# Kernel tuning notes

Measured on AMD Instinct MI355X. Metric: run time of the kernel, lower is better.

## Reference

```python
import jax, jax.numpy as jnp
import numpy as np

GROUP_SIZE = 128
INTERMEDIATE = 18944


def _unpack_int4(packed):
    # packed: [rows, cols//8] int32, 8 nibbles per int32 along output dim
    shifts = jnp.arange(8, dtype=jnp.int32) * 4
    nib = (packed[:, :, None] >> shifts) & 15  # [rows, cols//8, 8]
    return nib.reshape(packed.shape[0], packed.shape[1] * 8)


def awq_gemm(x, qweight, qzeros, scales, group_size):
    # Dequantize: W[i,j] = (w4[i,j] - z4[i//g, j]) * scales[i//g, j]
    w = _unpack_int4(qweight).astype(jnp.float32)           # [in, out]
    z = _unpack_int4(qzeros).astype(jnp.float32)            # [in//g, out]
    s = scales.astype(jnp.float32)                          # [in//g, out]
    W = ((w - jnp.repeat(z, group_size, axis=0)) * jnp.repeat(s, group_size, axis=0))
    return (x @ W.astype(x.dtype))                          # [tokens, out]


def setup_inputs() -> dict:
    key = jax.random.key(0)
    ks = jax.random.split(key, 7)
    imax = 2147483647
    return {
        "x": (jax.random.normal(ks[0], (4096, 3584), dtype=jnp.float32) * 0.02).astype(jnp.float16),
        "qweight_gu": jax.random.randint(ks[1], (3584, 4736), 0, imax, dtype=jnp.int32),
        "qzeros_gu": jax.random.randint(ks[2], (28, 4736), 0, imax, dtype=jnp.int32),
        "scales_gu": (jax.random.uniform(ks[3], (28, 37888), dtype=jnp.float32) * 0.01 + 0.001).astype(jnp.float16),
        "qweight_down": jax.random.randint(ks[4], (18944, 448), 0, imax, dtype=jnp.int32),
        "qzeros_down": jax.random.randint(ks[5], (148, 448), 0, imax, dtype=jnp.int32),
        "scales_down": (jax.random.uniform(ks[6], (148, 3584), dtype=jnp.float32) * 0.01 + 0.001).astype(jnp.float16),
    }


def reference(x, qweight_gu, qzeros_gu, scales_gu, qweight_down, qzeros_down, scales_down):
    # Fused gate+up AWQ GEMM (matches forward path after fuse_gate_up())
    gate_up = awq_gemm(x, qweight_gu, qzeros_gu, scales_gu, GROUP_SIZE)  # [T, 2*I]
    gate = gate_up[..., :INTERMEDIATE]
    up = gate_up[..., INTERMEDIATE:]
    intermediate = jax.nn.silu(gate) * up                                # fused SiLU*mul
    down = awq_gemm(intermediate, qweight_down, qzeros_down, scales_down, GROUP_SIZE)
    return down
```

## Files before the change

kernel.cpp:

```cpp
#include <hip/hip_runtime.h>
#include <hip/hip_fp16.h>
#include <stdint.h>

typedef _Float16 half8 __attribute__((ext_vector_type(8)));
typedef _Float16 h2v __attribute__((ext_vector_type(2)));
typedef float f32x4 __attribute__((ext_vector_type(4)));

#define GLD_LDS16(gp, lp)                                                     \
  __builtin_amdgcn_global_load_lds(                                           \
      (const __attribute__((address_space(1))) void*)(gp),                    \
      (__attribute__((address_space(3))) void*)(lp), 16, 0, 0)
#define GLD_LDS4(gp, lp)                                                      \
  __builtin_amdgcn_global_load_lds(                                           \
      (const __attribute__((address_space(1))) void*)(gp),                    \
      (__attribute__((address_space(3))) void*)(lp), 4, 0, 0)

__global__ void xcvt_kernel(const float* __restrict__ in, __half* __restrict__ out) {
  const size_t i = ((size_t)blockIdx.x * 256 + threadIdx.x) * 4;
  float4 v = *(const float4*)(in + i);
  __half2* o = (__half2*)(out + i);
  o[0] = __floats2half2_rn(v.x, v.y);
  o[1] = __floats2half2_rn(v.z, v.w);
}

__global__ void repack_kernel(const int* __restrict__ qw, uint32_t* __restrict__ rp, int P) {
  const int N = P * 8;
  const int n = blockIdx.x * 256 + threadIdx.x;
  const int j8 = n >> 3;
  const int sh = (n & 7) * 4;
  #pragma unroll
  for (int qi = 0; qi < 4; ++qi) {
    const int q = blockIdx.y * 4 + qi;
    const int* src = qw + (size_t)(q * 8) * P + j8;
    uint32_t r = 0;
    #pragma unroll
    for (int t = 0; t < 8; ++t) {
      uint32_t w = ((uint32_t)src[t * P] >> sh) & 15u;
      r |= w << (4 * (t >> 1) + 16 * (t & 1));
    }
    rp[(size_t)q * N + n] = r;
  }
}

__global__ void smz_kernel(const float* __restrict__ sc, const int* __restrict__ qz,
                           uint32_t* __restrict__ smz, int P) {
  const int N = P * 8;
  const int n = blockIdx.x * 256 + threadIdx.x;
  const int g = blockIdx.y;
  uint32_t sbits = __half_as_ushort(__float2half(sc[(size_t)g * N + n]));
  uint32_t z = ((uint32_t)qz[(size_t)g * P + (n >> 3)] >> ((n & 7) * 4)) & 15u;
  uint32_t hz = 0x6400u | z;
  smz[(size_t)g * N + n] = sbits | (hz << 16);
}

union U32H2 { uint32_t u; h2v h; };
__device__ inline h2v bith2(uint32_t u) { U32H2 t; t.u = u; return t.h; }
__device__ inline uint32_t h2bit(h2v h) { U32H2 t; t.h = h; return t.u; }
__device__ inline half8 dequant8(uint32_t p, h2v s, h2v z) {
  union { uint32_t u[4]; half8 v; } r;
  r.u[0] = h2bit((bith2((p & 0x000F000Fu) | 0x64006400u) - z) * s);
  r.u[1] = h2bit((bith2(((p >> 4) & 0x000F000Fu) | 0x64006400u) - z) * s);
  r.u[2] = h2bit((bith2(((p >> 8) & 0x000F000Fu) | 0x64006400u) - z) * s);
  r.u[3] = h2bit((bith2(((p >> 12) & 0x000F000Fu) | 0x64006400u) - z) * s);
  return r.v;
}

template <int KDIM, int NW, int T1OFF, int OW, bool SILU, int BXS>
__global__ __launch_bounds__(512, 4) void awq_gemm(const __half* __restrict__ A,
                                                   const uint32_t* __restrict__ RP,
                                                   const uint32_t* __restrict__ SMZ,
                                                   void* __restrict__ OUT) {
  constexpr int ABUF = 128 * 64 * 2;
  constexpr int BBUF = 8 * 256 * 4;
  constexpr int BOFF = 3 * ABUF;
  constexpr int ZOFF = BOFF + 3 * BBUF;
  __shared__ __align__(16) unsigned char smem[ZOFF + 2048];

  const int tid = threadIdx.x;
  const int l = tid & 63;
  const int wv = tid >> 6;
  const int l15 = l & 15;
  const int l4 = l >> 4;
  const int wc = wv * 16;

  const int row0 = blockIdx.y * 128;
  const int n0 = blockIdx.x * BXS;

  const __half* asrc[2];
  #pragma unroll
  for (int it = 0; it < 2; ++it) {
    int m = it * 64 + (tid >> 3);
    int cs = tid & 7;
    int kc = cs ^ (m & 7);
    asrc[it] = A + (size_t)(row0 + m) * KDIM + kc * 8;
  }

  const uint32_t* bsrc;
  {
    int qr = tid >> 6;
    int c4 = (tid & 63) * 4;
    int S = ((qr & 1) << 4) | ((qr >> 1) << 2);
    int cS = c4 ^ S;
    int bcol = (cS < 128) ? n0 + cS : n0 + T1OFF + (cS - 128);
    bsrc = RP + (size_t)qr * NW + bcol;
  }

  const uint32_t* zsrc;
  {
    int w3 = wv & 3;
    int zc = w3 * 64 + l;
    zsrc = SMZ + ((zc < 128) ? n0 + zc : n0 + T1OFF + (zc - 128));
  }
  const int zdst = ZOFF + (wv & 3) * 256;

  f32x4 acc0[8], acc1[8];
  const f32x4 zero4 = {0.f, 0.f, 0.f, 0.f};
  #pragma unroll
  for (int mf = 0; mf < 8; ++mf) { acc0[mf] = zero4; acc1[mf] = zero4; }

  uint32_t s2[2], z2[2];
  constexpr int NSTEP = KDIM / 64;

  #pragma unroll
  for (int it = 0; it < 2; ++it)
    GLD_LDS16(asrc[it], &smem[it * 8192 + tid * 16]);
  GLD_LDS16(bsrc, &smem[BOFF + tid * 16]);
  GLD_LDS4(zsrc, &smem[zdst]);
  #pragma unroll
  for (int it = 0; it < 2; ++it)
    GLD_LDS16(asrc[it] + 64, &smem[ABUF + it * 8192 + tid * 16]);
  GLD_LDS16(bsrc + (size_t)8 * NW, &smem[BOFF + BBUF + tid * 16]);

  int cur = 0, stg = 2;
  for (int t = 0; t < NSTEP; ++t) {
    if (t == NSTEP - 1)      asm volatile("s_waitcnt vmcnt(0)" ::: "memory");
    else if (t & 1)          asm volatile("s_waitcnt vmcnt(4)" ::: "memory");
    else                     asm volatile("s_waitcnt vmcnt(3)" ::: "memory");
    __builtin_amdgcn_s_barrier();

    if (t + 2 < NSTEP) {
      #pragma unroll
      for (int it = 0; it < 2; ++it)
        GLD_LDS16(asrc[it] + (size_t)(t + 2) * 64,
                  &smem[stg * ABUF + it * 8192 + tid * 16]);
      GLD_LDS16(bsrc + (size_t)(t + 2) * 8 * NW, &smem[BOFF + stg * BBUF + tid * 16]);
      if (((t + 2) & 1) == 0) {
        const int g = (t + 2) >> 1;
        GLD_LDS4(zsrc + (size_t)g * NW, &smem[zdst + (g & 1) * 1024]);
      }
    }

    if ((t & 1) == 0) {
      const uint32_t* zl = (const uint32_t*)&smem[ZOFF + ((t >> 1) & 1) * 1024];
      uint32_t u0 = zl[wc + l15];
      uint32_t u1 = zl[128 + wc + l15];
      uint32_t lo0 = u0 & 0xFFFFu, lo1 = u1 & 0xFFFFu;
      s2[0] = lo0 | (lo0 << 16);
      z2[0] = (u0 & 0xFFFF0000u) | (u0 >> 16);
      s2[1] = lo1 | (lo1 << 16);
      z2[1] = (u1 & 0xFFFF0000u) | (u1 >> 16);
    }

    uint32_t bq[2][2];
    const uint32_t* bdw = (const uint32_t*)&smem[BOFF + cur * BBUF];
    #pragma unroll
    for (int kk = 0; kk < 2; ++kk) {
      const int Sl = ((l4 & 1) << 4) | (kk << 3) | ((l4 >> 1) << 2);
      const int qrow = (kk * 4 + l4) * 256;
      bq[kk][0] = bdw[qrow + ((wc + l15) ^ Sl)];
      bq[kk][1] = bdw[qrow + ((128 + wc + l15) ^ Sl)];
    }

    const unsigned char* abase = &smem[cur * ABUF];
    __builtin_amdgcn_s_setprio(1);
    #pragma unroll
    for (int kk = 0; kk < 2; ++kk) {
      half8 b0 = dequant8(bq[kk][0], bith2(s2[0]), bith2(z2[0]));
      half8 b1 = dequant8(bq[kk][1], bith2(s2[1]), bith2(z2[1]));
      const int chunkoff = ((kk * 4 + l4) ^ (l15 & 7)) * 16;
      #pragma unroll
      for (int mf = 0; mf < 8; ++mf) {
        half8 a = *(const half8*)(abase + (mf * 16 + l15) * 128 + chunkoff);
        acc0[mf] = __builtin_amdgcn_mfma_f32_16x16x32_f16(a, b0, acc0[mf], 0, 0, 0);
        acc1[mf] = __builtin_amdgcn_mfma_f32_16x16x32_f16(a, b1, acc1[mf], 0, 0, 0);
      }
    }
    __builtin_amdgcn_s_setprio(0);

    cur = (cur == 2) ? 0 : cur + 1;
    stg = (stg == 2) ? 0 : stg + 1;
  }

  if (SILU) {
    __half* O = (__half*)OUT;
    #pragma unroll
    for (int mf = 0; mf < 8; ++mf)
      #pragma unroll
      for (int r = 0; r < 4; ++r) {
        int row = row0 + mf * 16 + l4 * 4 + r;
        int col = n0 + wc + l15;
        float gf = __half2float(__float2half(acc0[mf][r]));
        float uf = __half2float(__float2half(acc1[mf][r]));
        float sig = 1.f / (1.f + __expf(-gf));
        float sil = __half2float(__float2half(gf * sig));
        O[(size_t)row * OW + col] = __float2half(sil * uf);
      }
  } else {
    float* O = (float*)OUT;
    #pragma unroll
    for (int mf = 0; mf < 8; ++mf)
      #pragma unroll
      for (int r = 0; r < 4; ++r) {
        int row = row0 + mf * 16 + l4 * 4 + r;
        int col0 = n0 + wc + l15;
        int col1 = n0 + T1OFF + wc + l15;
        O[(size_t)row * OW + col0] = __half2float(__float2half(acc0[mf][r]));
        O[(size_t)row * OW + col1] = __half2float(__float2half(acc1[mf][r]));
      }
  }
}

extern "C" void kernel_launch(void* const* d_in, const int* in_sizes, int n_in,
                              void* d_out, int out_size, void* d_ws, size_t ws_size,
                              hipStream_t stream) {
  const float* x_f32 = (const float*)d_in[0];
  const int* qw_gu = (const int*)d_in[1];
  const int* qz_gu = (const int*)d_in[2];
  const float* sc_gu = (const float*)d_in[3];
  const int* qw_dn = (const int*)d_in[4];
  const int* qz_dn = (const int*)d_in[5];
  const float* sc_dn = (const float*)d_in[6];

  char* ws = (char*)d_ws;
  __half* interm   = (__half*)ws;
  uint32_t* rp_gu  = (uint32_t*)(ws + 155189248ull);
  uint32_t* smz_gu = (uint32_t*)(ws + 223084544ull);
  __half* xh       = (__half*)(ws + 227328000ull);
  uint32_t* rp_dn  = (uint32_t*)(ws + 155189248ull);
  uint32_t* smz_dn = (uint32_t*)(ws + 189136896ull);

  xcvt_kernel<<<14336, 256, 0, stream>>>(x_f32, xh);
  repack_kernel<<<dim3(148, 112), 256, 0, stream>>>(qw_gu, rp_gu, 4736);
  smz_kernel<<<dim3(148, 28), 256, 0, stream>>>(sc_gu, qz_gu, smz_gu, 4736);

  awq_gemm<3584, 37888, 18944, 18944, true, 128>
      <<<dim3(148, 32), 512, 0, stream>>>(xh, rp_gu, smz_gu, (void*)interm);

  repack_kernel<<<dim3(14, 592), 256, 0, stream>>>(qw_dn, rp_dn, 448);
  smz_kernel<<<dim3(14, 148), 256, 0, stream>>>(sc_dn, qz_dn, smz_dn, 448);

  awq_gemm<18944, 3584, 128, 3584, false, 256>
      <<<dim3(14, 32), 512, 0, stream>>>(interm, rp_dn, smz_dn, d_out);
}
```

Baseline: 1.630 ms.

## Enlarge M tile to 256 with 2x4 warp grid and phased barrier pipeline

Doubles the block's M tile to 256 rows and arranges the 8 warps as 2x4, each computing a 128x64 tile with 32 accumulators. Each dequantized weight fragment is reused across more MFMAs, which cuts dequant ALU work and LDS traffic per FLOP. The K-step is split into four barrier-separated phases that interleave global-to-LDS prefetch with MFMA work. The cost is higher register pressure (launch bounds lowered to 2 blocks/CU), more barriers, and half as many blocks, which may underfill the GPU for the down projection.

```diff
diff --git a/kernel.cpp b/kernel.cpp
--- a/kernel.cpp
+++ b/kernel.cpp
@@ -14,6 +14,8 @@
   __builtin_amdgcn_global_load_lds(                                           \
       (const __attribute__((address_space(1))) void*)(gp),                    \
       (__attribute__((address_space(3))) void*)(lp), 4, 0, 0)
+
+#define SBAR() asm volatile("s_barrier" ::: "memory")
 
 __global__ void xcvt_kernel(const float* __restrict__ in, __half* __restrict__ out) {
   const size_t i = ((size_t)blockIdx.x * 256 + threadIdx.x) * 4;
@@ -66,11 +68,11 @@
 }
 
 template <int KDIM, int NW, int T1OFF, int OW, bool SILU, int BXS>
-__global__ __launch_bounds__(512, 4) void awq_gemm(const __half* __restrict__ A,
+__global__ __launch_bounds__(512, 2) void awq_gemm(const __half* __restrict__ A,
                                                    const uint32_t* __restrict__ RP,
                                                    const uint32_t* __restrict__ SMZ,
                                                    void* __restrict__ OUT) {
-  constexpr int ABUF = 128 * 64 * 2;
+  constexpr int ABUF = 256 * 64 * 2;
   constexpr int BBUF = 8 * 256 * 4;
   constexpr int BOFF = 3 * ABUF;
   constexpr int ZOFF = BOFF + 3 * BBUF;
@@ -79,16 +81,18 @@
   const int tid = threadIdx.x;
   const int l = tid & 63;
   const int wv = tid >> 6;
+  const int wm = wv >> 2;
+  const int wn = wv & 3;
   const int l15 = l & 15;
   const int l4 = l >> 4;
-  const int wc = wv * 16;
-
-  const int row0 = blockIdx.y * 128;
+  const int l157 = l15 & 7;
+
+  const int row0 = blockIdx.y * 256;
   const int n0 = blockIdx.x * BXS;
 
-  const __half* asrc[2];
-  #pragma unroll
-  for (int it = 0; it < 2; ++it) {
+  const __half* asrc[4];
+  #pragma unroll
+  for (int it = 0; it < 4; ++it) {
     int m = it * 64 + (tid >> 3);
     int cs = tid & 7;
     int kc = cs ^ (m & 7);
@@ -107,85 +111,141 @@
 
   const uint32_t* zsrc;
   {
-    int w3 = wv & 3;
-    int zc = w3 * 64 + l;
+    int zc = tid & 255;
     zsrc = SMZ + ((zc < 128) ? n0 + zc : n0 + T1OFF + (zc - 128));
   }
-  const int zdst = ZOFF + (wv & 3) * 256;
-
-  f32x4 acc0[8], acc1[8];
+
+  int chi[4];
+  #pragma unroll
+  for (int nf = 0; nf < 4; ++nf)
+    chi[nf] = (nf >> 1) * 128 + wn * 32 + (nf & 1) * 16 + l15;
+  int arow[8];
+  #pragma unroll
+  for (int mf = 0; mf < 8; ++mf)
+    arow[mf] = (wm * 128 + mf * 16 + l15) * 128;
+
+  f32x4 acc[4][8];
   const f32x4 zero4 = {0.f, 0.f, 0.f, 0.f};
   #pragma unroll
-  for (int mf = 0; mf < 8; ++mf) { acc0[mf] = zero4; acc1[mf] = zero4; }
-
-  uint32_t s2[2], z2[2];
+  for (int nf = 0; nf < 4; ++nf)
+    #pragma unroll
+    for (int mf = 0; mf < 8; ++mf) acc[nf][mf] = zero4;
+
+  uint32_t s2[4], z2[4];
   constexpr int NSTEP = KDIM / 64;
 
   #pragma unroll
-  for (int it = 0; it < 2; ++it)
+  for (int it = 0; it < 4; ++it)
     GLD_LDS16(asrc[it], &smem[it * 8192 + tid * 16]);
   GLD_LDS16(bsrc, &smem[BOFF + tid * 16]);
-  GLD_LDS4(zsrc, &smem[zdst]);
-  #pragma unroll
-  for (int it = 0; it < 2; ++it)
+  GLD_LDS4(zsrc, &smem[ZOFF + (tid & 255) * 4]);
+  #pragma unroll
+  for (int it = 0; it < 4; ++it)
     GLD_LDS16(asrc[it] + 64, &smem[ABUF + it * 8192 + tid * 16]);
   GLD_LDS16(bsrc + (size_t)8 * NW, &smem[BOFF + BBUF + tid * 16]);
 
+  asm volatile("s_waitcnt vmcnt(5)" ::: "memory");
+  SBAR();
+
   int cur = 0, stg = 2;
   for (int t = 0; t < NSTEP; ++t) {
-    if (t == NSTEP - 1)      asm volatile("s_waitcnt vmcnt(0)" ::: "memory");
-    else if (t & 1)          asm volatile("s_waitcnt vmcnt(4)" ::: "memory");
-    else                     asm volatile("s_waitcnt vmcnt(3)" ::: "memory");
-    __builtin_amdgcn_s_barrier();
+    const int aoff = cur * ABUF;
+    uint32_t bq[4];
+    half8 afr[4], bfr[4];
+    const uint32_t* bdw = (const uint32_t*)&smem[BOFF + cur * BBUF];
+    const int Sl0 = ((l4 & 1) << 4) | ((l4 >> 1) << 2);
 
     if (t + 2 < NSTEP) {
-      #pragma unroll
-      for (int it = 0; it < 2; ++it)
-        GLD_LDS16(asrc[it] + (size_t)(t + 2) * 64,
-                  &smem[stg * ABUF + it * 8192 + tid * 16]);
+      GLD_LDS16(asrc[0] + (size_t)(t + 2) * 64, &smem[stg * ABUF + tid * 16]);
+      GLD_LDS16(asrc[1] + (size_t)(t + 2) * 64, &smem[stg * ABUF + 8192 + tid * 16]);
+    }
+    #pragma unroll
+    for (int nf = 0; nf < 4; ++nf)
+      bq[nf] = bdw[l4 * 256 + (chi[nf] ^ Sl0)];
+    if ((t & 1) == 0) {
+      const uint32_t* zl = (const uint32_t*)&smem[ZOFF + ((t >> 1) & 1) * 1024];
+      #pragma unroll
+      for (int nf = 0; nf < 4; ++nf) {
+        uint32_t u = zl[chi[nf]];
+        uint32_t lo = u & 0xFFFFu;
+        s2[nf] = lo | (lo << 16);
+        z2[nf] = (u & 0xFFFF0000u) | (u >> 16);
+      }
+    }
+    #pragma unroll
+    for (int i = 0; i < 4; ++i)
+      afr[i] = *(const half8*)&smem[aoff + arow[i] + (l4 ^ l157) * 16];
+    SBAR();
+    __builtin_amdgcn_s_setprio(1);
+    #pragma unroll
+    for (int nf = 0; nf < 4; ++nf)
+      bfr[nf] = dequant8(bq[nf], bith2(s2[nf]), bith2(z2[nf]));
+    #pragma unroll
+    for (int nf = 0; nf < 4; ++nf)
+      #pragma unroll
+      for (int i = 0; i < 4; ++i)
+        acc[nf][i] = __builtin_amdgcn_mfma_f32_16x16x32_f16(afr[i], bfr[nf], acc[nf][i], 0, 0, 0);
+    __builtin_amdgcn_s_setprio(0);
+    SBAR();
+
+    if (t + 2 < NSTEP) {
+      GLD_LDS16(asrc[2] + (size_t)(t + 2) * 64, &smem[stg * ABUF + 16384 + tid * 16]);
+      GLD_LDS16(asrc[3] + (size_t)(t + 2) * 64, &smem[stg * ABUF + 24576 + tid * 16]);
+    }
+    #pragma unroll
+    for (int i = 0; i < 4; ++i)
+      afr[i] = *(const half8*)&smem[aoff + arow[4 + i] + (l4 ^ l157) * 16];
+    SBAR();
+    __builtin_amdgcn_s_setprio(1);
+    #pragma unroll
+    for (int nf = 0; nf < 4; ++nf)
+      #pragma unroll
+      for (int i = 0; i < 4; ++i)
+        acc[nf][4 + i] = __builtin_amdgcn_mfma_f32_16x16x32_f16(afr[i], bfr[nf], acc[nf][4 + i], 0, 0, 0);
+    __builtin_amdgcn_s_setprio(0);
+    SBAR();
+
+    if (t + 2 < NSTEP) {
       GLD_LDS16(bsrc + (size_t)(t + 2) * 8 * NW, &smem[BOFF + stg * BBUF + tid * 16]);
       if (((t + 2) & 1) == 0) {
         const int g = (t + 2) >> 1;
-        GLD_LDS4(zsrc + (size_t)g * NW, &smem[zdst + (g & 1) * 1024]);
+        GLD_LDS4(zsrc + (size_t)g * NW, &smem[ZOFF + (g & 1) * 1024 + (tid & 255) * 4]);
       }
     }
-
-    if ((t & 1) == 0) {
-      const uint32_t* zl = (const uint32_t*)&smem[ZOFF + ((t >> 1) & 1) * 1024];
-      uint32_t u0 = zl[wc + l15];
-      uint32_t u1 = zl[128 + wc + l15];
-      uint32_t lo0 = u0 & 0xFFFFu, lo1 = u1 & 0xFFFFu;
-      s2[0] = lo0 | (lo0 << 16);
-      z2[0] = (u0 & 0xFFFF0000u) | (u0 >> 16);
-      s2[1] = lo1 | (lo1 << 16);
-      z2[1] = (u1 & 0xFFFF0000u) | (u1 >> 16);
-    }
-
-    uint32_t bq[2][2];
-    const uint32_t* bdw = (const uint32_t*)&smem[BOFF + cur * BBUF];
-    #pragma unroll
-    for (int kk = 0; kk < 2; ++kk) {
-      const int Sl = ((l4 & 1) << 4) | (kk << 3) | ((l4 >> 1) << 2);
-      const int qrow = (kk * 4 + l4) * 256;
-      bq[kk][0] = bdw[qrow + ((wc + l15) ^ Sl)];
-      bq[kk][1] = bdw[qrow + ((128 + wc + l15) ^ Sl)];
-    }
-
-    const unsigned char* abase = &smem[cur * ABUF];
+    #pragma unroll
+    for (int nf = 0; nf < 4; ++nf)
+      bq[nf] = bdw[(4 + l4) * 256 + (chi[nf] ^ (Sl0 | 8))];
+    #pragma unroll
+    for (int i = 0; i < 4; ++i)
+      afr[i] = *(const half8*)&smem[aoff + arow[i] + ((4 + l4) ^ l157) * 16];
+    SBAR();
     __builtin_amdgcn_s_setprio(1);
     #pragma unroll
-    for (int kk = 0; kk < 2; ++kk) {
-      half8 b0 = dequant8(bq[kk][0], bith2(s2[0]), bith2(z2[0]));
-      half8 b1 = dequant8(bq[kk][1], bith2(s2[1]), bith2(z2[1]));
-      const int chunkoff = ((kk * 4 + l4) ^ (l15 & 7)) * 16;
-      #pragma unroll
-      for (int mf = 0; mf < 8; ++mf) {
-        half8 a = *(const half8*)(abase + (mf * 16 + l15) * 128 + chunkoff);
-        acc0[mf] = __builtin_amdgcn_mfma_f32_16x16x32_f16(a, b0, acc0[mf], 0, 0, 0);
-        acc1[mf] = __builtin_amdgcn_mfma_f32_16x16x32_f16(a, b1, acc1[mf], 0, 0, 0);
-      }
-    }
+    for (int nf = 0; nf < 4; ++nf)
+      bfr[nf] = dequant8(bq[nf], bith2(s2[nf]), bith2(z2[nf]));
+    #pragma unroll
+    for (int nf = 0; nf < 4; ++nf)
+      #pragma unroll
+      for (int i = 0; i < 4; ++i)
+        acc[nf][i] = __builtin_amdgcn_mfma_f32_16x16x32_f16(afr[i], bfr[nf], acc[nf][i], 0, 0, 0);
     __builtin_amdgcn_s_setprio(0);
+    SBAR();
+
+    #pragma unroll
+    for (int i = 0; i < 4; ++i)
+      afr[i] = *(const half8*)&smem[aoff + arow[4 + i] + ((4 + l4) ^ l157) * 16];
+    SBAR();
+    __builtin_amdgcn_s_setprio(1);
+    #pragma unroll
+    for (int nf = 0; nf < 4; ++nf)
+      #pragma unroll
+      for (int i = 0; i < 4; ++i)
+        acc[nf][4 + i] = __builtin_amdgcn_mfma_f32_16x16x32_f16(afr[i], bfr[nf], acc[nf][4 + i], 0, 0, 0);
+    __builtin_amdgcn_s_setprio(0);
+    if (t + 2 >= NSTEP)      asm volatile("s_waitcnt vmcnt(0)" ::: "memory");
+    else if (t & 1)          asm volatile("s_waitcnt vmcnt(5)" ::: "memory");
+    else                     asm volatile("s_waitcnt vmcnt(6)" ::: "memory");
+    SBAR();
 
     cur = (cur == 2) ? 0 : cur + 1;
     stg = (stg == 2) ? 0 : stg + 1;
@@ -194,29 +254,31 @@
   if (SILU) {
     __half* O = (__half*)OUT;
     #pragma unroll
-    for (int mf = 0; mf < 8; ++mf)
-      #pragma unroll
-      for (int r = 0; r < 4; ++r) {
-        int row = row0 + mf * 16 + l4 * 4 + r;
-        int col = n0 + wc + l15;
-        float gf = __half2float(__float2half(acc0[mf][r]));
-        float uf = __half2float(__float2half(acc1[mf][r]));
-        float sig = 1.f / (1.f + __expf(-gf));
-        float sil = __half2float(__float2half(gf * sig));
-        O[(size_t)row * OW + col] = __float2half(sil * uf);
-      }
+    for (int nfg = 0; nfg < 2; ++nfg)
+      #pragma unroll
+      for (int mf = 0; mf < 8; ++mf)
+        #pragma unroll
+        for (int r = 0; r < 4; ++r) {
+          int row = row0 + wm * 128 + mf * 16 + l4 * 4 + r;
+          int col = n0 + wn * 32 + nfg * 16 + l15;
+          float gf = __half2float(__float2half(acc[nfg][mf][r]));
+          float uf = __half2float(__float2half(acc[2 + nfg][mf][r]));
+          float sig = 1.f / (1.f + __expf(-gf));
+          float sil = __half2float(__float2half(gf * sig));
+          O[(size_t)row * OW + col] = __float2half(sil * uf);
+        }
   } else {
     float* O = (float*)OUT;
     #pragma unroll
-    for (int mf = 0; mf < 8; ++mf)
-      #pragma unroll
-      for (int r = 0; r < 4; ++r) {
-        int row = row0 + mf * 16 + l4 * 4 + r;
-        int col0 = n0 + wc + l15;
-        int col1 = n0 + T1OFF + wc + l15;
-        O[(size_t)row * OW + col0] = __half2float(__float2half(acc0[mf][r]));
-        O[(size_t)row * OW + col1] = __half2float(__float2half(acc1[mf][r]));
-      }
+    for (int nf = 0; nf < 4; ++nf)
+      #pragma unroll
+      for (int mf = 0; mf < 8; ++mf)
+        #pragma unroll
+        for (int r = 0; r < 4; ++r) {
+          int row = row0 + wm * 128 + mf * 16 + l4 * 4 + r;
+          int col = n0 + (nf >> 1) * T1OFF + wn * 32 + (nf & 1) * 16 + l15;
+          O[(size_t)row * OW + col] = __half2float(__float2half(acc[nf][mf][r]));
+        }
   }
 }
 
@@ -244,11 +306,11 @@
   smz_kernel<<<dim3(148, 28), 256, 0, stream>>>(sc_gu, qz_gu, smz_gu, 4736);
 
   awq_gemm<3584, 37888, 18944, 18944, true, 128>
-      <<<dim3(148, 32), 512, 0, stream>>>(xh, rp_gu, smz_gu, (void*)interm);
+      <<<dim3(148, 16), 512, 0, stream>>>(xh, rp_gu, smz_gu, (void*)interm);
 
   repack_kernel<<<dim3(14, 592), 256, 0, stream>>>(qw_dn, rp_dn, 448);
   smz_kernel<<<dim3(14, 148), 256, 0, stream>>>(sc_dn, qz_dn, smz_dn, 448);
 
   awq_gemm<18944, 3584, 128, 3584, false, 256>
-      <<<dim3(14, 32), 512, 0, stream>>>(interm, rp_dn, smz_dn, d_out);
-}
+      <<<dim3(14, 16), 512, 0, stream>>>(interm, rp_dn, smz_dn, d_out);
+}
```

Result: slower. 1.820 ms (+11.6%).

## Use 256-row M tile for gate/up AWQ GEMM with 2x4 warp layout

Applied to the files above, without the earlier changes.

Adds an awq_gemm_big kernel that doubles the M tile to 256 rows and arranges the 8 waves as 2x4 (each wave covering 128 rows by 64 columns), and uses it for the gate/up GEMM with half as many row blocks. Each dequantized B fragment now feeds twice as many MFMAs, which cuts weight loads and dequant work per output and halves how often B is re-read from global memory. In exchange, LDS use and register pressure grow (32 accumulator vectors per lane, launch bounds lowered to 2 blocks per CU), so occupancy drops. The grid is also smaller, which may hurt load balance across CUs.

```diff
diff --git a/kernel.cpp b/kernel.cpp
--- a/kernel.cpp
+++ b/kernel.cpp
@@ -66,6 +66,180 @@
 }
 
 template <int KDIM, int NW, int T1OFF, int OW, bool SILU, int BXS>
+__global__ __launch_bounds__(512, 2) void awq_gemm_big(const __half* __restrict__ A,
+                                                       const uint32_t* __restrict__ RP,
+                                                       const uint32_t* __restrict__ SMZ,
+                                                       void* __restrict__ OUT) {
+  constexpr int ABUF = 256 * 64 * 2;
+  constexpr int BBUF = 8 * 256 * 4;
+  constexpr int BOFF = 3 * ABUF;
+  constexpr int ZOFF = BOFF + 3 * BBUF;
+  __shared__ __align__(16) unsigned char smem[ZOFF + 2048];
+
+  const int tid = threadIdx.x;
+  const int l = tid & 63;
+  const int wv = tid >> 6;
+  const int wm = wv >> 2;
+  const int wn = wv & 3;
+  const int l15 = l & 15;
+  const int l4 = l >> 4;
+  const int l157 = l15 & 7;
+
+  const int row0 = blockIdx.y * 256;
+  const int n0 = blockIdx.x * BXS;
+
+  const __half* asrc[4];
+  #pragma unroll
+  for (int it = 0; it < 4; ++it) {
+    int m = it * 64 + (tid >> 3);
+    int cs = tid & 7;
+    int kc = cs ^ (m & 7);
+    asrc[it] = A + (size_t)(row0 + m) * KDIM + kc * 8;
+  }
+
+  const uint32_t* bsrc;
+  {
+    int qr = tid >> 6;
+    int c4 = (tid & 63) * 4;
+    int S = ((qr & 1) << 4) | ((qr >> 1) << 2);
+    int cS = c4 ^ S;
+    int bcol = (cS < 128) ? n0 + cS : n0 + T1OFF + (cS - 128);
+    bsrc = RP + (size_t)qr * NW + bcol;
+  }
+
+  const uint32_t* zsrc;
+  {
+    int zc = tid & 255;
+    zsrc = SMZ + ((zc < 128) ? n0 + zc : n0 + T1OFF + (zc - 128));
+  }
+
+  int chi[4];
+  #pragma unroll
+  for (int nf = 0; nf < 4; ++nf)
+    chi[nf] = (nf >> 1) * 128 + wn * 32 + (nf & 1) * 16 + l15;
+  int arow[8];
+  #pragma unroll
+  for (int mf = 0; mf < 8; ++mf)
+    arow[mf] = (wm * 128 + mf * 16 + l15) * 128;
+
+  f32x4 acc[4][8];
+  const f32x4 zero4 = {0.f, 0.f, 0.f, 0.f};
+  #pragma unroll
+  for (int nf = 0; nf < 4; ++nf)
+    #pragma unroll
+    for (int mf = 0; mf < 8; ++mf) acc[nf][mf] = zero4;
+
+  uint32_t s2[4], z2[4];
+  constexpr int NSTEP = KDIM / 64;
+
+  #pragma unroll
+  for (int it = 0; it < 4; ++it)
+    GLD_LDS16(asrc[it], &smem[it * 8192 + tid * 16]);
+  GLD_LDS16(bsrc, &smem[BOFF + tid * 16]);
+  GLD_LDS4(zsrc, &smem[ZOFF + (tid & 255) * 4]);
+  #pragma unroll
+  for (int it = 0; it < 4; ++it)
+    GLD_LDS16(asrc[it] + 64, &smem[ABUF + it * 8192 + tid * 16]);
+  GLD_LDS16(bsrc + (size_t)8 * NW, &smem[BOFF + BBUF + tid * 16]);
+
+  int cur = 0, stg = 2;
+  for (int t = 0; t < NSTEP; ++t) {
+    if (t == NSTEP - 1)      asm volatile("s_waitcnt vmcnt(0)" ::: "memory");
+    else if (t & 1)          asm volatile("s_waitcnt vmcnt(6)" ::: "memory");
+    else                     asm volatile("s_waitcnt vmcnt(5)" ::: "memory");
+    __builtin_amdgcn_s_barrier();
+
+    if (t + 2 < NSTEP) {
+      #pragma unroll
+      for (int it = 0; it < 4; ++it)
+        GLD_LDS16(asrc[it] + (size_t)(t + 2) * 64,
+                  &smem[stg * ABUF + it * 8192 + tid * 16]);
+      GLD_LDS16(bsrc + (size_t)(t + 2) * 8 * NW, &smem[BOFF + stg * BBUF + tid * 16]);
+      if (((t + 2) & 1) == 0) {
+        const int g = (t + 2) >> 1;
+        GLD_LDS4(zsrc + (size_t)g * NW, &smem[ZOFF + (g & 1) * 1024 + (tid & 255) * 4]);
+      }
+    }
+
+    if ((t & 1) == 0) {
+      const uint32_t* zl = (const uint32_t*)&smem[ZOFF + ((t >> 1) & 1) * 1024];
+      #pragma unroll
+      for (int nf = 0; nf < 4; ++nf) {
+        uint32_t u = zl[chi[nf]];
+        uint32_t lo = u & 0xFFFFu;
+        s2[nf] = lo | (lo << 16);
+        z2[nf] = (u & 0xFFFF0000u) | (u >> 16);
+      }
+    }
+
+    uint32_t bq[2][4];
+    const uint32_t* bdw = (const uint32_t*)&smem[BOFF + cur * BBUF];
+    #pragma unroll
+    for (int kk = 0; kk < 2; ++kk) {
+      const int Sl = ((l4 & 1) << 4) | (kk << 3) | ((l4 >> 1) << 2);
+      #pragma unroll
+      for (int nf = 0; nf < 4; ++nf)
+        bq[kk][nf] = bdw[(kk * 4 + l4) * 256 + (chi[nf] ^ Sl)];
+    }
+
+    const unsigned char* abase = &smem[cur * ABUF];
+    __builtin_amdgcn_s_setprio(1);
+    #pragma unroll
+    for (int kk = 0; kk < 2; ++kk) {
+      const int coff = ((kk * 4 + l4) ^ l157) * 16;
+      half8 afr[8];
+      #pragma unroll
+      for (int mf = 0; mf < 8; ++mf)
+        afr[mf] = *(const half8*)&smem[(size_t)(abase - smem) + arow[mf] + coff];
+      half8 bfr[4];
+      #pragma unroll
+      for (int nf = 0; nf < 4; ++nf)
+        bfr[nf] = dequant8(bq[kk][nf], bith2(s2[nf]), bith2(z2[nf]));
+      #pragma unroll
+      for (int nf = 0; nf < 4; ++nf)
+        #pragma unroll
+        for (int mf = 0; mf < 8; ++mf)
+          acc[nf][mf] =
+              __builtin_amdgcn_mfma_f32_16x16x32_f16(afr[mf], bfr[nf], acc[nf][mf], 0, 0, 0);
+    }
+    __builtin_amdgcn_s_setprio(0);
+
+    cur = (cur == 2) ? 0 : cur + 1;
+    stg = (stg == 2) ? 0 : stg + 1;
+  }
+
+  if (SILU) {
+    __half* O = (__half*)OUT;
+    #pragma unroll
+    for (int nfg = 0; nfg < 2; ++nfg)
+      #pragma unroll
+      for (int mf = 0; mf < 8; ++mf)
+        #pragma unroll
+        for (int r = 0; r < 4; ++r) {
+          int row = row0 + wm * 128 + mf * 16 + l4 * 4 + r;
+          int col = n0 + wn * 32 + nfg * 16 + l15;
+          float gf = __half2float(__float2half(acc[nfg][mf][r]));
+          float uf = __half2float(__float2half(acc[2 + nfg][mf][r]));
+          float sig = 1.f / (1.f + __expf(-gf));
+          float sil = __half2float(__float2half(gf * sig));
+          O[(size_t)row * OW + col] = __float2half(sil * uf);
+        }
+  } else {
+    float* O = (float*)OUT;
+    #pragma unroll
+    for (int nf = 0; nf < 4; ++nf)
+      #pragma unroll
+      for (int mf = 0; mf < 8; ++mf)
+        #pragma unroll
+        for (int r = 0; r < 4; ++r) {
+          int row = row0 + wm * 128 + mf * 16 + l4 * 4 + r;
+          int col = n0 + (nf >> 1) * T1OFF + wn * 32 + (nf & 1) * 16 + l15;
+          O[(size_t)row * OW + col] = __half2float(__float2half(acc[nf][mf][r]));
+        }
+  }
+}
+
+template <int KDIM, int NW, int T1OFF, int OW, bool SILU, int BXS>
 __global__ __launch_bounds__(512, 4) void awq_gemm(const __half* __restrict__ A,
                                                    const uint32_t* __restrict__ RP,
                                                    const uint32_t* __restrict__ SMZ,
@@ -243,8 +417,8 @@
   repack_kernel<<<dim3(148, 112), 256, 0, stream>>>(qw_gu, rp_gu, 4736);
   smz_kernel<<<dim3(148, 28), 256, 0, stream>>>(sc_gu, qz_gu, smz_gu, 4736);
 
-  awq_gemm<3584, 37888, 18944, 18944, true, 128>
-      <<<dim3(148, 32), 512, 0, stream>>>(xh, rp_gu, smz_gu, (void*)interm);
+  awq_gemm_big<3584, 37888, 18944, 18944, true, 128>
+      <<<dim3(148, 16), 512, 0, stream>>>(xh, rp_gu, smz_gu, (void*)interm);
 
   repack_kernel<<<dim3(14, 592), 256, 0, stream>>>(qw_dn, rp_dn, 448);
   smz_kernel<<<dim3(14, 148), 256, 0, stream>>>(sc_dn, qz_dn, smz_dn, 448);
```

Measured after the change: 1.683 ms. 3.3% more time.

## Switch AWQ GEMM to 32x32x16 MFMA with k-major A layout in LDS

Applied to the files above, without the earlier changes.

Replaces the 16x16x32 MFMA tiling, where each wave covered 16 gate and 16 up columns, with 32x32x16 MFMA tiles where each wave owns 32 output columns. The A tile is stored in LDS in a k-chunk-major layout without the XOR swizzle, and the B and zero-point loads are simplified to match. Each wave now dequantizes fewer B values per step and does fewer, larger MFMAs. In exchange, the SiLU epilogue has to pass the up results through shared memory between waves with extra barriers. The unswizzled A layout may cause LDS bank conflicts.

```diff
diff --git a/kernel.cpp b/kernel.cpp
--- a/kernel.cpp
+++ b/kernel.cpp
@@ -4,7 +4,7 @@
 
 typedef _Float16 half8 __attribute__((ext_vector_type(8)));
 typedef _Float16 h2v __attribute__((ext_vector_type(2)));
-typedef float f32x4 __attribute__((ext_vector_type(4)));
+typedef float f32x16 __attribute__((ext_vector_type(16)));
 
 #define GLD_LDS16(gp, lp)                                                     \
   __builtin_amdgcn_global_load_lds(                                           \
@@ -70,7 +70,7 @@
                                                    const uint32_t* __restrict__ RP,
                                                    const uint32_t* __restrict__ SMZ,
                                                    void* __restrict__ OUT) {
-  constexpr int ABUF = 128 * 64 * 2;
+  constexpr int ABUF = 8 * 128 * 16;
   constexpr int BBUF = 8 * 256 * 4;
   constexpr int BOFF = 3 * ABUF;
   constexpr int ZOFF = BOFF + 3 * BBUF;
@@ -79,53 +79,48 @@
   const int tid = threadIdx.x;
   const int l = tid & 63;
   const int wv = tid >> 6;
-  const int l15 = l & 15;
-  const int l4 = l >> 4;
-  const int wc = wv * 16;
+  const int l31 = l & 31;
+  const int lh = l >> 5;
 
   const int row0 = blockIdx.y * 128;
   const int n0 = blockIdx.x * BXS;
 
   const __half* asrc[2];
   #pragma unroll
-  for (int it = 0; it < 2; ++it) {
-    int m = it * 64 + (tid >> 3);
-    int cs = tid & 7;
-    int kc = cs ^ (m & 7);
-    asrc[it] = A + (size_t)(row0 + m) * KDIM + kc * 8;
-  }
+  for (int it = 0; it < 2; ++it)
+    asrc[it] = A + (size_t)(row0 + (tid & 127)) * KDIM + (it * 4 + (tid >> 7)) * 8;
 
   const uint32_t* bsrc;
   {
     int qr = tid >> 6;
     int c4 = (tid & 63) * 4;
-    int S = ((qr & 1) << 4) | ((qr >> 1) << 2);
-    int cS = c4 ^ S;
-    int bcol = (cS < 128) ? n0 + cS : n0 + T1OFF + (cS - 128);
+    int bcol = (c4 < 128) ? n0 + c4 : n0 + T1OFF + (c4 - 128);
     bsrc = RP + (size_t)qr * NW + bcol;
   }
 
   const uint32_t* zsrc;
   {
-    int w3 = wv & 3;
-    int zc = w3 * 64 + l;
+    int zc = tid & 255;
     zsrc = SMZ + ((zc < 128) ? n0 + zc : n0 + T1OFF + (zc - 128));
   }
-  const int zdst = ZOFF + (wv & 3) * 256;
-
-  f32x4 acc0[8], acc1[8];
-  const f32x4 zero4 = {0.f, 0.f, 0.f, 0.f};
-  #pragma unroll
-  for (int mf = 0; mf < 8; ++mf) { acc0[mf] = zero4; acc1[mf] = zero4; }
-
-  uint32_t s2[2], z2[2];
+
+  f32x16 acc[4];
+  #pragma unroll
+  for (int rf = 0; rf < 4; ++rf)
+    #pragma unroll
+    for (int e = 0; e < 16; ++e) acc[rf][e] = 0.f;
+
+  uint32_t s2, z2;
   constexpr int NSTEP = KDIM / 64;
+
+  const int bidx = wv * 32 + l31;
+  const int arow16 = l31 * 16;
 
   #pragma unroll
   for (int it = 0; it < 2; ++it)
     GLD_LDS16(asrc[it], &smem[it * 8192 + tid * 16]);
   GLD_LDS16(bsrc, &smem[BOFF + tid * 16]);
-  GLD_LDS4(zsrc, &smem[zdst]);
+  GLD_LDS4(zsrc, &smem[ZOFF + (tid & 255) * 4]);
   #pragma unroll
   for (int it = 0; it < 2; ++it)
     GLD_LDS16(asrc[it] + 64, &smem[ABUF + it * 8192 + tid * 16]);
@@ -146,43 +141,34 @@
       GLD_LDS16(bsrc + (size_t)(t + 2) * 8 * NW, &smem[BOFF + stg * BBUF + tid * 16]);
       if (((t + 2) & 1) == 0) {
         const int g = (t + 2) >> 1;
-        GLD_LDS4(zsrc + (size_t)g * NW, &smem[zdst + (g & 1) * 1024]);
+        GLD_LDS4(zsrc + (size_t)g * NW, &smem[ZOFF + (g & 1) * 1024 + (tid & 255) * 4]);
       }
     }
 
     if ((t & 1) == 0) {
       const uint32_t* zl = (const uint32_t*)&smem[ZOFF + ((t >> 1) & 1) * 1024];
-      uint32_t u0 = zl[wc + l15];
-      uint32_t u1 = zl[128 + wc + l15];
-      uint32_t lo0 = u0 & 0xFFFFu, lo1 = u1 & 0xFFFFu;
-      s2[0] = lo0 | (lo0 << 16);
-      z2[0] = (u0 & 0xFFFF0000u) | (u0 >> 16);
-      s2[1] = lo1 | (lo1 << 16);
-      z2[1] = (u1 & 0xFFFF0000u) | (u1 >> 16);
-    }
-
-    uint32_t bq[2][2];
+      uint32_t u = zl[bidx];
+      uint32_t lo = u & 0xFFFFu;
+      s2 = lo | (lo << 16);
+      z2 = (u & 0xFFFF0000u) | (u >> 16);
+    }
+
+    uint32_t bq[4];
     const uint32_t* bdw = (const uint32_t*)&smem[BOFF + cur * BBUF];
     #pragma unroll
-    for (int kk = 0; kk < 2; ++kk) {
-      const int Sl = ((l4 & 1) << 4) | (kk << 3) | ((l4 >> 1) << 2);
-      const int qrow = (kk * 4 + l4) * 256;
-      bq[kk][0] = bdw[qrow + ((wc + l15) ^ Sl)];
-      bq[kk][1] = bdw[qrow + ((128 + wc + l15) ^ Sl)];
-    }
+    for (int kf = 0; kf < 4; ++kf)
+      bq[kf] = bdw[(kf * 2 + lh) * 256 + bidx];
 
     const unsigned char* abase = &smem[cur * ABUF];
     __builtin_amdgcn_s_setprio(1);
     #pragma unroll
-    for (int kk = 0; kk < 2; ++kk) {
-      half8 b0 = dequant8(bq[kk][0], bith2(s2[0]), bith2(z2[0]));
-      half8 b1 = dequant8(bq[kk][1], bith2(s2[1]), bith2(z2[1]));
-      const int chunkoff = ((kk * 4 + l4) ^ (l15 & 7)) * 16;
-      #pragma unroll
-      for (int mf = 0; mf < 8; ++mf) {
-        half8 a = *(const half8*)(abase + (mf * 16 + l15) * 128 + chunkoff);
-        acc0[mf] = __builtin_amdgcn_mfma_f32_16x16x32_f16(a, b0, acc0[mf], 0, 0, 0);
-        acc1[mf] = __builtin_amdgcn_mfma_f32_16x16x32_f16(a, b1, acc1[mf], 0, 0, 0);
+    for (int kf = 0; kf < 4; ++kf) {
+      half8 b = dequant8(bq[kf], bith2(s2), bith2(z2));
+      const int coff = (kf * 2 + lh) * 2048 + arow16;
+      #pragma unroll
+      for (int rf = 0; rf < 4; ++rf) {
+        half8 a = *(const half8*)(abase + coff + rf * 512);
+        acc[rf] = __builtin_amdgcn_mfma_f32_32x32x16_f16(a, b, acc[rf], 0, 0, 0);
       }
     }
     __builtin_amdgcn_s_setprio(0);
@@ -192,30 +178,44 @@
   }
 
   if (SILU) {
-    __half* O = (__half*)OUT;
-    #pragma unroll
-    for (int mf = 0; mf < 8; ++mf)
-      #pragma unroll
-      for (int r = 0; r < 4; ++r) {
-        int row = row0 + mf * 16 + l4 * 4 + r;
-        int col = n0 + wc + l15;
-        float gf = __half2float(__float2half(acc0[mf][r]));
-        float uf = __half2float(__float2half(acc1[mf][r]));
-        float sig = 1.f / (1.f + __expf(-gf));
-        float sil = __half2float(__float2half(gf * sig));
-        O[(size_t)row * OW + col] = __float2half(sil * uf);
-      }
+    __half* uph = (__half*)smem;
+    __syncthreads();
+    if (wv >= 4) {
+      const int col = (wv - 4) * 32 + l31;
+      #pragma unroll
+      for (int rf = 0; rf < 4; ++rf)
+        #pragma unroll
+        for (int reg = 0; reg < 16; ++reg) {
+          int row = rf * 32 + (reg & 3) + 8 * (reg >> 2) + 4 * lh;
+          uph[row * 128 + col] = __float2half(acc[rf][reg]);
+        }
+    }
+    __syncthreads();
+    if (wv < 4) {
+      __half* O = (__half*)OUT;
+      const int col = wv * 32 + l31;
+      #pragma unroll
+      for (int rf = 0; rf < 4; ++rf)
+        #pragma unroll
+        for (int reg = 0; reg < 16; ++reg) {
+          int row = rf * 32 + (reg & 3) + 8 * (reg >> 2) + 4 * lh;
+          float gf = __half2float(__float2half(acc[rf][reg]));
+          float uf = __half2float(uph[row * 128 + col]);
+          float sig = 1.f / (1.f + __expf(-gf));
+          float sil = __half2float(__float2half(gf * sig));
+          O[(size_t)(row0 + row) * OW + n0 + col] = __float2half(sil * uf);
+        }
+    }
   } else {
     float* O = (float*)OUT;
-    #pragma unroll
-    for (int mf = 0; mf < 8; ++mf)
-      #pragma unroll
-      for (int r = 0; r < 4; ++r) {
-        int row = row0 + mf * 16 + l4 * 4 + r;
-        int col0 = n0 + wc + l15;
-        int col1 = n0 + T1OFF + wc + l15;
-        O[(size_t)row * OW + col0] = __half2float(__float2half(acc0[mf][r]));
-        O[(size_t)row * OW + col1] = __half2float(__float2half(acc1[mf][r]));
+    const int colc = bidx;
+    const int col = (colc < 128) ? n0 + colc : n0 + T1OFF + (colc - 128);
+    #pragma unroll
+    for (int rf = 0; rf < 4; ++rf)
+      #pragma unroll
+      for (int reg = 0; reg < 16; ++reg) {
+        int row = rf * 32 + (reg & 3) + 8 * (reg >> 2) + 4 * lh;
+        O[(size_t)(row0 + row) * OW + col] = __half2float(__float2half(acc[rf][reg]));
       }
   }
 }
```

After: 1.819 ms. +11.6%, slower.
